# Kernel tuning notes

Measured on AMD Instinct MI355X. Metric: run time of the kernel, lower is better.

## Reference

```python
import jax, jax.numpy as jnp
import numpy as np

B, S, D = 2, 2048, 2048
H, KV, HD = 32, 8, 64  # num_heads, num_kv_heads, head_dim
NREP = H // KV


def rotate_half(x):
    x1, x2 = x[..., : x.shape[-1] // 2], x[..., x.shape[-1] // 2 :]
    return jnp.concatenate((-x2, x1), axis=-1)


def setup_inputs() -> dict:
    key = jax.random.key(0)
    ks = jax.random.split(key, 5)
    x = jax.random.normal(ks[0], (B, S, D), dtype=jnp.float32)
    # weights stored as [in, out] so y = x @ W (same math as nn.Linear with random init)
    Wq = jax.random.normal(ks[1], (D, D), dtype=jnp.float32) * (D ** -0.5)
    Wk = jax.random.normal(ks[2], (D, KV * HD), dtype=jnp.float32) * (D ** -0.5)
    Wv = jax.random.normal(ks[3], (D, KV * HD), dtype=jnp.float32) * (D ** -0.5)
    Wo = jax.random.normal(ks[4], (D, D), dtype=jnp.float32) * (D ** -0.5)
    # standard RoPE tables, broadcastable over [B, H, S, HD]
    inv_freq = 1.0 / (10000.0 ** (jnp.arange(0, HD, 2, dtype=jnp.float32) / HD))
    freqs = jnp.arange(S, dtype=jnp.float32)[:, None] * inv_freq[None, :]  # [S, HD/2]
    emb = jnp.concatenate((freqs, freqs), axis=-1)  # [S, HD]
    cos = jnp.cos(emb)[None, None]  # [1,1,S,HD]
    sin = jnp.sin(emb)[None, None]
    # causal mask, masked where == 0
    attention_mask = jnp.tril(jnp.ones((S, S), dtype=jnp.int32))[None, None]
    return {"x": x, "cos": cos, "sin": sin, "Wq": Wq, "Wk": Wk, "Wv": Wv,
            "Wo": Wo, "attention_mask": attention_mask}


def reference(x, cos, sin, Wq, Wk, Wv, Wo, attention_mask):
    b, s, _ = x.shape
    q = (x @ Wq).reshape(b, s, H, HD).transpose(0, 2, 1, 3)   # [B,H,S,HD]
    k = (x @ Wk).reshape(b, s, KV, HD).transpose(0, 2, 1, 3)  # [B,KV,S,HD]
    v = (x @ Wv).reshape(b, s, KV, HD).transpose(0, 2, 1, 3)  # [B,KV,S,HD]
    # RoPE (elementwise) commutes with head-repeat; apply before grouping
    q = q * cos + rotate_half(q) * sin
    k = k * cos + rotate_half(k) * sin
    # GQA head broadcast instead of repeat_interleave: group q as [B,KV,NREP,S,HD]
    qg = q.reshape(b, KV, NREP, s, HD)
    scores = jnp.einsum('bgrqd,bgkd->bgrqk', qg, k) / jnp.sqrt(jnp.float32(HD))
    scores = jnp.where(attention_mask[:, :, None] == 0, jnp.float32(-1e9), scores)
    probs = jax.nn.softmax(scores, axis=-1)
    out = jnp.einsum('bgrqk,bgkd->bgrqd', probs, v)           # [B,KV,NREP,S,HD]
    out = out.reshape(b, H, s, HD).transpose(0, 2, 1, 3).reshape(b, s, H * HD)
    return out @ Wo
```

## Files before the change

kernel.cpp:

```cpp
#include <hip/hip_runtime.h>
#include <hip/hip_bf16.h>
#include <stdint.h>

#define B_ 2
#define S_ 2048
#define D_ 2048
#define H_ 32
#define KV_ 8
#define HD_ 64
#define NQKV 3072

typedef __bf16 bf16_t;
typedef __bf16 bf16x8 __attribute__((ext_vector_type(8)));
typedef __bf16 bf16x4 __attribute__((ext_vector_type(4)));
typedef float  f32x4  __attribute__((ext_vector_type(4)));
typedef float  f32x16 __attribute__((ext_vector_type(16)));
typedef unsigned int u32;
typedef u32 u32x4 __attribute__((ext_vector_type(4)));

typedef const __attribute__((address_space(1))) uint32_t* gp1_t;
typedef __attribute__((address_space(3))) uint32_t* lp3_t;

__device__ inline void gload_lds16(const void* g, void* l) {
  __builtin_amdgcn_global_load_lds((gp1_t)(uintptr_t)g, (lp3_t)(uint32_t)(uintptr_t)l,
                                   16, 0, 0);
}

__device__ inline u32 pkbf(float a, float b) {
  union { bf16_t h[2]; u32 u; } v;
  v.h[0] = (bf16_t)a; v.h[1] = (bf16_t)b;
  return v.u;
}

__device__ inline void pl32swap(u32 &a, u32 &b) {
  asm("v_permlane32_swap_b32 %0, %1" : "+v"(a), "+v"(b));
}

__global__ void cvt_f32_bf16(const float* __restrict__ in, bf16_t* __restrict__ out, int n4) {
  int i = blockIdx.x * blockDim.x + threadIdx.x;
  if (i < n4) {
    float4 v = ((const float4*)in)[i];
    bf16x4 o;
    o[0] = (bf16_t)v.x; o[1] = (bf16_t)v.y; o[2] = (bf16_t)v.z; o[3] = (bf16_t)v.w;
    ((bf16x4*)out)[i] = o;
  }
}

__global__ void transpose_cvt(const float* __restrict__ in, bf16_t* __restrict__ out,
                              int C, int row_off) {
  __shared__ float t[32][33];
  int tx = threadIdx.x, ty = threadIdx.y;
  int c0 = blockIdx.x * 32, r0 = blockIdx.y * 32;
#pragma unroll
  for (int j = 0; j < 4; ++j)
    t[ty + j*8][tx] = in[(int64_t)(r0 + ty + j*8) * C + c0 + tx];
  __syncthreads();
#pragma unroll
  for (int j = 0; j < 4; ++j)
    out[(int64_t)(row_off + c0 + ty + j*8) * 2048 + r0 + tx] = (bf16_t)t[tx][ty + j*8];
}

__global__ void v_transpose(const bf16_t* __restrict__ qkv, bf16_t* __restrict__ Vt) {
  __shared__ bf16_t t[32][34];
  const int tx = threadIdx.x, ty = threadIdx.y;
  const int c0 = blockIdx.x * 32;
  const int s0 = blockIdx.y * 32;
  const int b  = blockIdx.z;
#pragma unroll
  for (int j = 0; j < 4; ++j)
    t[ty + j*8][tx] = qkv[(int64_t)(b * S_ + s0 + ty + j*8) * NQKV + 2560 + c0 + tx];
  __syncthreads();
#pragma unroll
  for (int j = 0; j < 4; ++j)
    Vt[(int64_t)(b * 512 + c0 + ty + j*8) * S_ + s0 + tx] = t[tx][ty + j*8];
}

#define QSCALE 0.18033688011112042f
__global__ __launch_bounds__(256) void rope_scatter2(const bf16_t* __restrict__ qkv,
                                                     const float* __restrict__ cosb,
                                                     const float* __restrict__ sinb,
                                                     bf16_t* __restrict__ Q,
                                                     bf16_t* __restrict__ Kr) {
  const int row = blockIdx.x;
  const int b = row >> 11, s = row & 2047;
  const bf16_t* src = qkv + (int64_t)row * NQKV;
  const float* cs = cosb + s * HD_;
  const float* sn = sinb + s * HD_;
  const int tid = threadIdx.x;
  {
    const int c0 = tid * 8;
    const int d0 = c0 & 63, h = c0 >> 6;
    bf16x8 own = *(const bf16x8*)(src + c0);
    bf16x8 par = *(const bf16x8*)(src + (c0 ^ 32));
    const float sgn = (d0 & 32) ? 1.f : -1.f;
    bf16x8 o;
#pragma unroll
    for (int j = 0; j < 8; ++j) {
      const int d = d0 + j;
      float val = (float)own[j] * cs[d] + sgn * (float)par[j] * sn[d];
      o[j] = (bf16_t)(val * QSCALE);
    }
    *(bf16x8*)(Q + ((int64_t)(b * H_ + h) * S_ + s) * HD_ + d0) = o;
  }
  if (tid < 64) {
    const int c0 = 2048 + tid * 8;
    const int d0 = (tid * 8) & 63, kvh = tid >> 3;
    bf16x8 own = *(const bf16x8*)(src + c0);
    bf16x8 par = *(const bf16x8*)(src + (c0 ^ 32));
    const float sgn = (d0 & 32) ? 1.f : -1.f;
    bf16x8 o;
#pragma unroll
    for (int j = 0; j < 8; ++j) {
      const int d = d0 + j;
      float val = (float)own[j] * cs[d] + sgn * (float)par[j] * sn[d];
      o[j] = (bf16_t)val;
    }
    *(bf16x8*)(Kr + ((int64_t)(b * KV_ + kvh) * S_ + s) * HD_ + d0) = o;
  }
}

template <int BN, int EPI, typename OutT>
__global__ __launch_bounds__(512, 2) void gemm256(const bf16_t* __restrict__ A,
                                                  const bf16_t* __restrict__ Bt,
                                                  OutT* __restrict__ Cout,
                                                  int N, int K) {
  constexpr int NB = BN / 64;
  constexpr int LT = 4 + NB;
  constexpr int WCOLS = BN / 4;
  constexpr int NF = WCOLS / 16;

  __shared__ bf16_t As[2][256 * 64];
  __shared__ bf16_t Bs[2][BN * 64];

  const int tid = threadIdx.x;
  const int w = tid >> 6, lane = tid & 63;
  const int l15 = lane & 15, l4 = lane >> 4;
  const int wr = w >> 2, wc = w & 3;
  const int bm = blockIdx.y * 256, bn = blockIdx.x * BN;

  const int rw = w * 8 + (lane >> 3);
  const int srcg = ((lane & 7) ^ ((lane >> 3) & 7)) << 3;
  const bf16_t* PA[4];
  const bf16_t* PB[NB];
#pragma unroll
  for (int L = 0; L < 4; ++L)
    PA[L] = A + (int64_t)(bm + L * 64 + rw) * K + srcg;
#pragma unroll
  for (int L = 0; L < NB; ++L)
    PB[L] = Bt + (int64_t)(bn + L * 64 + rw) * K + srcg;

  const int NK = K >> 6;
  const int xr = l15 & 7;
  const int g0 = (l4 ^ xr) << 3;
  const int g1 = ((4 + l4) ^ xr) << 3;

  f32x4 acc[8][NF] = {};

  auto stage = [&](int s, int buf, int toff) {
    if (s < 4) gload_lds16(PA[s] + toff, &As[buf][s * 4096 + w * 512]);
    else       gload_lds16(PB[s - 4] + toff, &Bs[buf][(s - 4) * 4096 + w * 512]);
  };

#pragma unroll
  for (int s = 0; s < LT; ++s) stage(s, 0, 0);
  asm volatile("s_waitcnt vmcnt(0)" ::: "memory");
  __syncthreads();

  for (int t = 0; t < NK; ++t) {
    const int p = t & 1;
    const bool more = (t + 1) < NK;
    const int toff = (t + 1) << 6;
    const bf16_t* Ab = &As[p][0];
    const bf16_t* Bb = &Bs[p][0];

    bf16x8 ball[NF][2];
#pragma unroll
    for (int nn = 0; nn < NF; ++nn) {
      const int rb = wc * WCOLS + nn * 16 + l15;
      ball[nn][0] = *(const bf16x8*)(Bb + rb * 64 + g0);
      ball[nn][1] = *(const bf16x8*)(Bb + rb * 64 + g1);
    }

#pragma unroll
    for (int mh = 0; mh < 2; ++mh) {
      if (more) {
        const int sb = mh * (LT / 2);
        const int se = (mh == 0) ? (LT / 2) : LT;
#pragma unroll
        for (int s = sb; s < se; ++s) stage(s, p ^ 1, toff);
      }
      bf16x8 af[4][2];
#pragma unroll
      for (int mm = 0; mm < 4; ++mm) {
        const int ra = wr * 128 + (mh * 4 + mm) * 16 + l15;
        af[mm][0] = *(const bf16x8*)(Ab + ra * 64 + g0);
        af[mm][1] = *(const bf16x8*)(Ab + ra * 64 + g1);
      }
      __builtin_amdgcn_s_setprio(1);
#pragma unroll
      for (int mm = 0; mm < 4; ++mm)
#pragma unroll
        for (int nn = 0; nn < NF; ++nn) {
          acc[mh*4+mm][nn] = __builtin_amdgcn_mfma_f32_16x16x32_bf16(
              af[mm][0], ball[nn][0], acc[mh*4+mm][nn], 0, 0, 0);
          acc[mh*4+mm][nn] = __builtin_amdgcn_mfma_f32_16x16x32_bf16(
              af[mm][1], ball[nn][1], acc[mh*4+mm][nn], 0, 0, 0);
        }
      __builtin_amdgcn_s_setprio(0);
    }
    if (more) {
      asm volatile("s_waitcnt vmcnt(0)" ::: "memory");
      __syncthreads();
    }
  }

#pragma unroll
  for (int m = 0; m < 8; ++m) {
    const int row = bm + wr * 128 + m * 16 + l4 * 4;
#pragma unroll
    for (int n = 0; n < NF; ++n) {
      const int col = bn + wc * WCOLS + n * 16 + l15;
#pragma unroll
      for (int r = 0; r < 4; ++r)
        Cout[(int64_t)(row + r) * N + col] = (OutT)acc[m][n][r];
    }
  }
}

#define SHIFT_ 8.0f
__global__ __launch_bounds__(256, 2) void attn7(const bf16_t* __restrict__ Q,
                                                const bf16_t* __restrict__ Kr,
                                                const bf16_t* __restrict__ Vt,
                                                bf16_t* __restrict__ AO) {
  const int bk = blockIdx.x;
  const int b = bk >> 3, kvh = bk & 7;
  const int y = blockIdx.y;
  const int q0A = y * 32, q0B = (63 - y) * 32;
  const int tid = threadIdx.x;
  const int w = tid >> 6, lane = tid & 63;
  const int l31 = lane & 31, hi = lane >> 5;
  const int h = kvh * 4 + w;

  __shared__ __align__(16) bf16_t Ks[3][64 * 64];
  __shared__ __align__(16) bf16_t Vs[3][64 * 64];

  const bf16_t* Kg = Kr + (int64_t)(b * KV_ + kvh) * S_ * HD_;
  const bf16_t* Vg = Vt + (int64_t)(b * KV_ + kvh) * HD_ * S_;

  const int rL = (w << 3) + (lane >> 3);
  const int sgr = ((lane & 7) ^ (rL & 7)) << 3;
  const bf16_t* Ksrc = Kg + (int64_t)rL * HD_ + sgr;
  const bf16_t* Vsrc = Vg + (int64_t)rL * S_ + sgr;

  const int NT = (63 - y) / 2 + 1;

  auto stage = [&](int t) {
    const int tc = (t < NT) ? t : (NT - 1);
    char* Kd = (char*)Ks + (t % 3) * 8192 + w * 1024;
    char* Vd = (char*)Vs + (t % 3) * 8192 + w * 1024;
    gload_lds16(Ksrc + (int64_t)tc * 64 * HD_, Kd);
    gload_lds16(Ksrc + (int64_t)(tc * 64 + 32) * HD_, Kd + 4096);
    gload_lds16(Vsrc + tc * 64, Vd);
    gload_lds16(Vsrc + (int64_t)32 * S_ + tc * 64, Vd + 4096);
  };

  const bf16_t* QbA = Q + ((int64_t)(b * H_ + h) * S_ + q0A) * HD_;
  const bf16_t* QbB = Q + ((int64_t)(b * H_ + h) * S_ + q0B) * HD_;
  bf16x8 qfA[4], qfB[4];
#pragma unroll
  for (int ds = 0; ds < 4; ++ds) {
    qfA[ds] = *(const bf16x8*)(QbA + l31 * HD_ + ds * 16 + hi * 8);
    qfB[ds] = *(const bf16x8*)(QbB + l31 * HD_ + ds * 16 + hi * 8);
  }

  f32x16 aA0 = {}, aA1 = {}, aB0 = {}, aB1 = {};
  float lhA = 0.f, lhB = 0.f;
  const int xorb = l31 & 7;

  const f32x16 sinit = {-SHIFT_, -SHIFT_, -SHIFT_, -SHIFT_,
                        -SHIFT_, -SHIFT_, -SHIFT_, -SHIFT_,
                        -SHIFT_, -SHIFT_, -SHIFT_, -SHIFT_,
                        -SHIFT_, -SHIFT_, -SHIFT_, -SHIFT_};

  auto softmax_pack = [&](const f32x16 &sacc, bool diag, float &lh,
                          bf16x8 &pf0, bf16x8 &pf1) {
    float p[16];
#pragma unroll
    for (int r = 0; r < 16; ++r) {
      float sc = sacc[r];
      if (diag) {
        int kvpos = (r & 3) + 8 * (r >> 2) + 4 * hi;
        if (kvpos > l31) sc = -1e30f;
      }
      p[r] = __builtin_amdgcn_exp2f(sc);
    }
    float t0 = (p[0] + p[1]) + (p[2] + p[3]);
    float t1 = (p[4] + p[5]) + (p[6] + p[7]);
    float t2 = (p[8] + p[9]) + (p[10] + p[11]);
    float t3 = (p[12] + p[13]) + (p[14] + p[15]);
    lh += (t0 + t1) + (t2 + t3);
    u32 pk[8];
#pragma unroll
    for (int i = 0; i < 8; ++i) pk[i] = pkbf(p[2*i], p[2*i+1]);
    u32 a0 = pk[0], b0 = pk[2]; pl32swap(a0, b0);
    u32 a1 = pk[1], b1 = pk[3]; pl32swap(a1, b1);
    u32 a2 = pk[4], b2 = pk[6]; pl32swap(a2, b2);
    u32 a3 = pk[5], b3 = pk[7]; pl32swap(a3, b3);
    pf0 = __builtin_bit_cast(bf16x8, (u32x4){a0, a1, b0, b1});
    pf1 = __builtin_bit_cast(bf16x8, (u32x4){a2, a3, b2, b3});
  };

  stage(0);
  stage(1);

  for (int t = 0; t < NT; ++t) {
    asm volatile("s_waitcnt vmcnt(4)" ::: "memory");
    __syncthreads();
    stage(t + 2);
    const char* KsB = (const char*)Ks + (t % 3) * 8192;
    const char* VsB = (const char*)Vs + (t % 3) * 8192;
#pragma unroll
    for (int sub = 0; sub < 2; ++sub) {
      const int kvbase = t * 64 + sub * 32;
      if (kvbase <= q0B) {
        const bool actA = (kvbase <= q0A);
        const char* Kbase = KsB + (sub * 32 + l31) * 128;
        bf16x8 kf[4];
#pragma unroll
        for (int ds = 0; ds < 4; ++ds)
          kf[ds] = *(const bf16x8*)(Kbase + ((((ds << 1) + hi) ^ xorb) << 4));
        f32x16 sA = sinit, sB = sinit;
        __builtin_amdgcn_s_setprio(1);
#pragma unroll
        for (int ds = 0; ds < 4; ++ds)
          sB = __builtin_amdgcn_mfma_f32_32x32x16_bf16(kf[ds], qfB[ds], sB, 0, 0, 0);
        if (actA) {
#pragma unroll
          for (int ds = 0; ds < 4; ++ds)
            sA = __builtin_amdgcn_mfma_f32_32x32x16_bf16(kf[ds], qfA[ds], sA, 0, 0, 0);
        }
        __builtin_amdgcn_s_setprio(0);
        bf16x8 pA0, pA1, pB0, pB1;
        softmax_pack(sB, kvbase == q0B, lhB, pB0, pB1);
        if (actA) softmax_pack(sA, kvbase == q0A, lhA, pA0, pA1);
        const char* Vb0 = VsB + l31 * 128;
        const char* Vb1 = VsB + (32 + l31) * 128;
        const int c0 = (sub << 2) + hi;
        const int c1 = c0 + 2;
        bf16x8 v00 = *(const bf16x8*)(Vb0 + ((c0 ^ xorb) << 4));
        bf16x8 v01 = *(const bf16x8*)(Vb0 + ((c1 ^ xorb) << 4));
        bf16x8 v10 = *(const bf16x8*)(Vb1 + ((c0 ^ xorb) << 4));
        bf16x8 v11 = *(const bf16x8*)(Vb1 + ((c1 ^ xorb) << 4));
        __builtin_amdgcn_s_setprio(1);
        aB0 = __builtin_amdgcn_mfma_f32_32x32x16_bf16(v00, pB0, aB0, 0, 0, 0);
        aB1 = __builtin_amdgcn_mfma_f32_32x32x16_bf16(v10, pB0, aB1, 0, 0, 0);
        aB0 = __builtin_amdgcn_mfma_f32_32x32x16_bf16(v01, pB1, aB0, 0, 0, 0);
        aB1 = __builtin_amdgcn_mfma_f32_32x32x16_bf16(v11, pB1, aB1, 0, 0, 0);
        if (actA) {
          aA0 = __builtin_amdgcn_mfma_f32_32x32x16_bf16(v00, pA0, aA0, 0, 0, 0);
          aA1 = __builtin_amdgcn_mfma_f32_32x32x16_bf16(v10, pA0, aA1, 0, 0, 0);
          aA0 = __builtin_amdgcn_mfma_f32_32x32x16_bf16(v01, pA1, aA0, 0, 0, 0);
          aA1 = __builtin_amdgcn_mfma_f32_32x32x16_bf16(v11, pA1, aA1, 0, 0, 0);
        }
        __builtin_amdgcn_s_setprio(0);
      }
    }
  }

  asm volatile("s_waitcnt vmcnt(0)" ::: "memory");

  auto epi = [&](const f32x16 &a0, const f32x16 &a1, float lh, int q0) {
    float l = lh + __shfl_xor(lh, 32);
    const float rl = 1.f / l;
    const int64_t row = (int64_t)(b * S_ + q0 + l31);
#pragma unroll
    for (int dt = 0; dt < 2; ++dt) {
#pragma unroll
      for (int g = 0; g < 4; ++g) {
        bf16x4 ov;
#pragma unroll
        for (int j = 0; j < 4; ++j) {
          float val = (dt ? a1[4*g + j] : a0[4*g + j]) * rl;
          ov[j] = (bf16_t)val;
        }
        const int d0 = dt * 32 + g * 8 + hi * 4;
        *(bf16x4*)(AO + row * D_ + h * HD_ + d0) = ov;
      }
    }
  };
  epi(aA0, aA1, lhA, q0A);
  epi(aB0, aB1, lhB, q0B);
}

extern "C" void kernel_launch(void* const* d_in, const int* in_sizes, int n_in,
                              void* d_out, int out_size, void* d_ws, size_t ws_size,
                              hipStream_t stream) {
  const float* x    = (const float*)d_in[0];
  const float* cosb = (const float*)d_in[1];
  const float* sinb = (const float*)d_in[2];
  const float* Wq   = (const float*)d_in[3];
  const float* Wk   = (const float*)d_in[4];
  const float* Wv   = (const float*)d_in[5];
  const float* Wo   = (const float*)d_in[6];
  float* out = (float*)d_out;

  bf16_t* ws = (bf16_t*)d_ws;
  size_t o = 0;
  bf16_t* xb    = ws + o; o += (size_t)4096 * 2048;
  bf16_t* Wqkvt = ws + o; o += (size_t)3072 * 2048;
  bf16_t* Wot   = ws + o; o += (size_t)2048 * 2048;
  bf16_t* qkv   = ws + o; o += (size_t)4096 * 3072;
  bf16_t* Qr    = ws + o; o += (size_t)B_ * H_ * S_ * HD_;
  bf16_t* Krb   = ws + o; o += (size_t)B_ * KV_ * S_ * HD_;
  bf16_t* Vtb   = ws + o; o += (size_t)B_ * KV_ * S_ * HD_;
  bf16_t* AO    = ws + o; o += (size_t)4096 * 2048;

  cvt_f32_bf16<<<(8388608/4 + 255)/256, 256, 0, stream>>>(x, xb, 8388608/4);
  transpose_cvt<<<dim3(2048/32, 2048/32), dim3(32, 8), 0, stream>>>(Wq, Wqkvt, 2048, 0);
  transpose_cvt<<<dim3(512/32, 2048/32),  dim3(32, 8), 0, stream>>>(Wk, Wqkvt, 512, 2048);
  transpose_cvt<<<dim3(512/32, 2048/32),  dim3(32, 8), 0, stream>>>(Wv, Wqkvt, 512, 2560);
  transpose_cvt<<<dim3(2048/32, 2048/32), dim3(32, 8), 0, stream>>>(Wo, Wot, 2048, 0);
  gemm256<192, 2, bf16_t><<<dim3(3072/192, 4096/256), 512, 0, stream>>>(
      xb, Wqkvt, qkv, 3072, 2048);
  rope_scatter2<<<4096, 256, 0, stream>>>(qkv, cosb, sinb, Qr, Krb);
  v_transpose<<<dim3(16, 64, 2), dim3(32, 8), 0, stream>>>(qkv, Vtb);
  attn7<<<dim3(16, 32), 256, 0, stream>>>(Qr, Krb, Vtb, AO);
  gemm256<128, 0, float><<<dim3(2048/128, 4096/256), 512, 0, stream>>>(
      AO, Wot, out, 2048, 2048);
}
```

Before: 180.2 us.

## Compute softmax row sums via MFMA with ones and swizzle GEMM block order

The attention kernel no longer sums probabilities with scalar adds. It adds extra MFMAs that multiply a vector of ones by the packed bf16 probabilities to get the row-sum denominator, which removes VALU adds and the cross-lane shuffle. The softmax for tile A is now interleaved after tile B's PV MFMAs to overlap work. The GEMM kernel also remaps block indices with an XCD-style swizzle (stride 8) to improve L2 locality. Trade-offs: two extra MFMAs per tile, and the denominator is computed from bf16-rounded probabilities, which makes it consistent with the numerator but less precise.

```diff
diff --git a/kernel.cpp b/kernel.cpp
--- a/kernel.cpp
+++ b/kernel.cpp
@@ -136,7 +136,12 @@
   const int w = tid >> 6, lane = tid & 63;
   const int l15 = lane & 15, l4 = lane >> 4;
   const int wr = w >> 2, wc = w & 3;
-  const int bm = blockIdx.y * 256, bn = blockIdx.x * BN;
+
+  const int nX = gridDim.x;
+  const int lin = blockIdx.y * nX + blockIdx.x;
+  const int cpx = (nX * gridDim.y) >> 3;
+  const int swz = (lin & 7) * cpx + (lin >> 3);
+  const int bm = (swz / nX) * 256, bn = (swz % nX) * BN;
 
   const int rw = w * 8 + (lane >> 3);
   const int srcg = ((lane & 7) ^ ((lane >> 3) & 7)) << 3;
@@ -228,7 +233,7 @@
 }
 
 #define SHIFT_ 8.0f
-__global__ __launch_bounds__(256, 2) void attn7(const bf16_t* __restrict__ Q,
+__global__ __launch_bounds__(256, 2) void attn8(const bf16_t* __restrict__ Q,
                                                 const bf16_t* __restrict__ Kr,
                                                 const bf16_t* __restrict__ Vt,
                                                 bf16_t* __restrict__ AO) {
@@ -273,8 +278,12 @@
     qfB[ds] = *(const bf16x8*)(QbB + l31 * HD_ + ds * 16 + hi * 8);
   }
 
+  bf16x8 onesf;
+#pragma unroll
+  for (int i = 0; i < 8; ++i) onesf[i] = (bf16_t)1.0f;
+
   f32x16 aA0 = {}, aA1 = {}, aB0 = {}, aB1 = {};
-  float lhA = 0.f, lhB = 0.f;
+  f32x16 lA = {}, lB = {};
   const int xorb = l31 & 7;
 
   const f32x16 sinit = {-SHIFT_, -SHIFT_, -SHIFT_, -SHIFT_,
@@ -282,7 +291,7 @@
                         -SHIFT_, -SHIFT_, -SHIFT_, -SHIFT_,
                         -SHIFT_, -SHIFT_, -SHIFT_, -SHIFT_};
 
-  auto softmax_pack = [&](const f32x16 &sacc, bool diag, float &lh,
+  auto softmax_pack = [&](const f32x16 &sacc, bool diag,
                           bf16x8 &pf0, bf16x8 &pf1) {
     float p[16];
 #pragma unroll
@@ -294,11 +303,6 @@
       }
       p[r] = __builtin_amdgcn_exp2f(sc);
     }
-    float t0 = (p[0] + p[1]) + (p[2] + p[3]);
-    float t1 = (p[4] + p[5]) + (p[6] + p[7]);
-    float t2 = (p[8] + p[9]) + (p[10] + p[11]);
-    float t3 = (p[12] + p[13]) + (p[14] + p[15]);
-    lh += (t0 + t1) + (t2 + t3);
     u32 pk[8];
 #pragma unroll
     for (int i = 0; i < 8; ++i) pk[i] = pkbf(p[2*i], p[2*i+1]);
@@ -340,9 +344,6 @@
             sA = __builtin_amdgcn_mfma_f32_32x32x16_bf16(kf[ds], qfA[ds], sA, 0, 0, 0);
         }
         __builtin_amdgcn_s_setprio(0);
-        bf16x8 pA0, pA1, pB0, pB1;
-        softmax_pack(sB, kvbase == q0B, lhB, pB0, pB1);
-        if (actA) softmax_pack(sA, kvbase == q0A, lhA, pA0, pA1);
         const char* Vb0 = VsB + l31 * 128;
         const char* Vb1 = VsB + (32 + l31) * 128;
         const int c0 = (sub << 2) + hi;
@@ -351,27 +352,36 @@
         bf16x8 v01 = *(const bf16x8*)(Vb0 + ((c1 ^ xorb) << 4));
         bf16x8 v10 = *(const bf16x8*)(Vb1 + ((c0 ^ xorb) << 4));
         bf16x8 v11 = *(const bf16x8*)(Vb1 + ((c1 ^ xorb) << 4));
+        bf16x8 pB0, pB1;
+        softmax_pack(sB, kvbase == q0B, pB0, pB1);
         __builtin_amdgcn_s_setprio(1);
         aB0 = __builtin_amdgcn_mfma_f32_32x32x16_bf16(v00, pB0, aB0, 0, 0, 0);
         aB1 = __builtin_amdgcn_mfma_f32_32x32x16_bf16(v10, pB0, aB1, 0, 0, 0);
         aB0 = __builtin_amdgcn_mfma_f32_32x32x16_bf16(v01, pB1, aB0, 0, 0, 0);
         aB1 = __builtin_amdgcn_mfma_f32_32x32x16_bf16(v11, pB1, aB1, 0, 0, 0);
+        lB  = __builtin_amdgcn_mfma_f32_32x32x16_bf16(onesf, pB0, lB, 0, 0, 0);
+        lB  = __builtin_amdgcn_mfma_f32_32x32x16_bf16(onesf, pB1, lB, 0, 0, 0);
+        __builtin_amdgcn_s_setprio(0);
         if (actA) {
+          bf16x8 pA0, pA1;
+          softmax_pack(sA, kvbase == q0A, pA0, pA1);
+          __builtin_amdgcn_s_setprio(1);
           aA0 = __builtin_amdgcn_mfma_f32_32x32x16_bf16(v00, pA0, aA0, 0, 0, 0);
           aA1 = __builtin_amdgcn_mfma_f32_32x32x16_bf16(v10, pA0, aA1, 0, 0, 0);
           aA0 = __builtin_amdgcn_mfma_f32_32x32x16_bf16(v01, pA1, aA0, 0, 0, 0);
           aA1 = __builtin_amdgcn_mfma_f32_32x32x16_bf16(v11, pA1, aA1, 0, 0, 0);
+          lA  = __builtin_amdgcn_mfma_f32_32x32x16_bf16(onesf, pA0, lA, 0, 0, 0);
+          lA  = __builtin_amdgcn_mfma_f32_32x32x16_bf16(onesf, pA1, lA, 0, 0, 0);
+          __builtin_amdgcn_s_setprio(0);
         }
-        __builtin_amdgcn_s_setprio(0);
       }
     }
   }
 
   asm volatile("s_waitcnt vmcnt(0)" ::: "memory");
 
-  auto epi = [&](const f32x16 &a0, const f32x16 &a1, float lh, int q0) {
-    float l = lh + __shfl_xor(lh, 32);
-    const float rl = 1.f / l;
+  auto epi = [&](const f32x16 &a0, const f32x16 &a1, float denom, int q0) {
+    const float rl = 1.f / denom;
     const int64_t row = (int64_t)(b * S_ + q0 + l31);
 #pragma unroll
     for (int dt = 0; dt < 2; ++dt) {
@@ -388,8 +398,8 @@
       }
     }
   };
-  epi(aA0, aA1, lhA, q0A);
-  epi(aB0, aB1, lhB, q0B);
+  epi(aA0, aA1, lA[0], q0A);
+  epi(aB0, aB1, lB[0], q0B);
 }
 
 extern "C" void kernel_launch(void* const* d_in, const int* in_sizes, int n_in,
@@ -424,7 +434,7 @@
       xb, Wqkvt, qkv, 3072, 2048);
   rope_scatter2<<<4096, 256, 0, stream>>>(qkv, cosb, sinb, Qr, Krb);
   v_transpose<<<dim3(16, 64, 2), dim3(32, 8), 0, stream>>>(qkv, Vtb);
-  attn7<<<dim3(16, 32), 256, 0, stream>>>(Qr, Krb, Vtb, AO);
+  attn8<<<dim3(16, 32), 256, 0, stream>>>(Qr, Krb, Vtb, AO);
   gemm256<128, 0, float><<<dim3(2048/128, 4096/256), 512, 0, stream>>>(
       AO, Wot, out, 2048, 2048);
 }
```

Result: no change. 178.8 us (-0.8%).
